# Kernel tuning notes

Hardware: AMD Instinct MI355X
Metric: run time of the kernel (lower is better)

## Reference

```python
import jax, jax.numpy as jnp
import numpy as np

EPS = 1e-3  # keras BatchNormalization default epsilon
NUM_HEADS = 8


def conv1d_same(x, w, b):
    # x: [B,T,Cin], w: [K,Cin,Cout]
    return jax.lax.conv_general_dilated(
        x, w, window_strides=(1,), padding='SAME',
        dimension_numbers=('NWC', 'WIO', 'NWC')) + b


def bn(x, g, b, m, v):
    # inference-mode batchnorm with moving stats
    return (x - m) * jax.lax.rsqrt(v + EPS) * g + b


def lstm(x, K, R, b):
    # x: [B,T,D] -> [B,T,U]; keras gate order i,f,c,o; recurrent_dropout off at inference
    B = x.shape[0]
    U = R.shape[0]
    xp = jnp.einsum('btd,dz->btz', x, K) + b  # precompute input projection

    def step(carry, xt):
        h, c = carry
        z = xt + h @ R
        i, f, g, o = jnp.split(z, 4, axis=-1)
        c = jax.nn.sigmoid(f) * c + jax.nn.sigmoid(i) * jnp.tanh(g)
        h = jax.nn.sigmoid(o) * jnp.tanh(c)
        return (h, c), h

    h0 = jnp.zeros((B, U), x.dtype)
    _, hs = jax.lax.scan(step, (h0, h0), jnp.swapaxes(xp, 0, 1))
    return jnp.swapaxes(hs, 0, 1)


def bilstm(x, Kf, Rf, bf, Kb, Rb, bb):
    fwd = lstm(x, Kf, Rf, bf)
    bwd = lstm(x[:, ::-1], Kb, Rb, bb)[:, ::-1]
    return jnp.concatenate([fwd, bwd], axis=-1)


def mhsa(x, wq, bq, wk, bk, wv, bv, wo, bo):
    B, T, _ = x.shape
    d_model = wq.shape[1]
    dh = d_model // NUM_HEADS
    q = (x @ wq + bq).reshape(B, T, NUM_HEADS, dh)
    k = (x @ wk + bk).reshape(B, T, NUM_HEADS, dh)
    v = (x @ wv + bv).reshape(B, T, NUM_HEADS, dh)
    logits = jnp.einsum('bqhd,bkhd->bhqk', q, k) / jnp.sqrt(jnp.asarray(dh, x.dtype))
    attn = jax.nn.softmax(logits, axis=-1)
    out = jnp.einsum('bhqk,bkhd->bqhd', attn, v).reshape(B, T, d_model)
    return out @ wo + bo


def setup_inputs() -> dict:
    key = jax.random.key(0)
    ks = iter(jax.random.split(key, 64))

    def nrm(shape, s=0.05):
        return (jax.random.normal(next(ks), shape) * s).astype(jnp.float32)

    p = {}
    p['x'] = jax.random.normal(next(ks), (512, 256, 78), dtype=jnp.float32)
    for name, shp in [
            ('conv5_w', (5, 78, 64)), ('conv7_w', (7, 78, 64)), ('conv9_w', (9, 78, 64)),
            ('fuse_w', (1, 192, 128)), ('se_w1', (128, 8)), ('se_w2', (8, 128)),
            ('l1f_k', (128, 512)), ('l1f_r', (128, 512)), ('l1b_k', (128, 512)), ('l1b_r', (128, 512)),
            ('l2f_k', (256, 256)), ('l2f_r', (64, 256)), ('l2b_k', (256, 256)), ('l2b_r', (64, 256)),
            ('wq', (128, 256)), ('wk', (128, 256)), ('wv', (128, 256)), ('wo', (256, 256)),
            ('d1_w', (256, 256)), ('d2_w', (256, 128)), ('d3_w', (128, 1)),
            ('conv5_b', (64,)), ('conv7_b', (64,)), ('conv9_b', (64,)), ('fuse_b', (128,)),
            ('se_b1', (8,)), ('se_b2', (128,)),
            ('l1f_b', (512,)), ('l1b_b', (512,)), ('l2f_b', (256,)), ('l2b_b', (256,)),
            ('bq', (256,)), ('bk', (256,)), ('bv', (256,)), ('bo', (256,)),
            ('d1_b', (256,)), ('d2_b', (128,)), ('d3_b', (1,))]:
        p[name] = nrm(shp)
    for tag, c in [('bn5', 64), ('bn7', 64), ('bn9', 64), ('bn_l1', 256),
                   ('bn_l2', 128), ('bn_d1', 256), ('bn_d2', 128)]:
        p[tag + '_g'] = jnp.ones((c,), jnp.float32)
        p[tag + '_b'] = jnp.zeros((c,), jnp.float32)
        p[tag + '_m'] = jnp.zeros((c,), jnp.float32)
        p[tag + '_v'] = jnp.ones((c,), jnp.float32)
    return p


def reference(x, conv5_w, conv5_b, bn5_g, bn5_b, bn5_m, bn5_v,
              conv7_w, conv7_b, bn7_g, bn7_b, bn7_m, bn7_v,
              conv9_w, conv9_b, bn9_g, bn9_b, bn9_m, bn9_v,
              fuse_w, fuse_b, se_w1, se_b1, se_w2, se_b2,
              l1f_k, l1f_r, l1f_b, l1b_k, l1b_r, l1b_b,
              bn_l1_g, bn_l1_b, bn_l1_m, bn_l1_v,
              l2f_k, l2f_r, l2f_b, l2b_k, l2b_r, l2b_b,
              bn_l2_g, bn_l2_b, bn_l2_m, bn_l2_v,
              wq, bq, wk, bk, wv, bv, wo, bo,
              d1_w, d1_b, bn_d1_g, bn_d1_b, bn_d1_m, bn_d1_v,
              d2_w, d2_b, bn_d2_g, bn_d2_b, bn_d2_m, bn_d2_v,
              d3_w, d3_b):
    def block(w, b, g, bt, m, v):
        h = jax.nn.relu(conv1d_same(x, w, b))
        h = bn(h, g, bt, m, v)
        B, T, C = h.shape  # MaxPooling1D(2, 'same'); T is even
        return h.reshape(B, T // 2, 2, C).max(axis=2)

    fused = jnp.concatenate([
        block(conv5_w, conv5_b, bn5_g, bn5_b, bn5_m, bn5_v),
        block(conv7_w, conv7_b, bn7_g, bn7_b, bn7_m, bn7_v),
        block(conv9_w, conv9_b, bn9_g, bn9_b, bn9_m, bn9_v)], axis=-1)
    fused = conv1d_same(fused, fuse_w, fuse_b)

    # SENet spatial attention
    s = fused.mean(axis=1)
    e = jax.nn.sigmoid(jax.nn.relu(s @ se_w1 + se_b1) @ se_w2 + se_b2)
    h = fused * e[:, None, :]

    h = bilstm(h, l1f_k, l1f_r, l1f_b, l1b_k, l1b_r, l1b_b)
    h = bn(h, bn_l1_g, bn_l1_b, bn_l1_m, bn_l1_v)
    h = bilstm(h, l2f_k, l2f_r, l2f_b, l2b_k, l2b_r, l2b_b)
    h = bn(h, bn_l2_g, bn_l2_b, bn_l2_m, bn_l2_v)

    h = mhsa(h, wq, bq, wk, bk, wv, bv, wo, bo)
    g_ = h.mean(axis=1)

    d = jax.nn.relu(g_ @ d1_w + d1_b)
    d = bn(d, bn_d1_g, bn_d1_b, bn_d1_m, bn_d1_v)
    d = jax.nn.relu(d @ d2_w + d2_b)
    d = bn(d, bn_d2_g, bn_d2_b, bn_d2_m, bn_d2_v)
    return jax.nn.sigmoid(d @ d3_w + d3_b)
```

## Files before the change

kernel.cpp:

```cpp
#include <hip/hip_runtime.h>

#define EPS 1e-3f

typedef __attribute__((ext_vector_type(8))) short bf16x8;
typedef __attribute__((ext_vector_type(4))) float f32x4;

__device__ __forceinline__ float sigm(float x){ return 1.0f/(1.0f + __expf(-x)); }
__device__ __forceinline__ float tanhfast(float x){ return 1.0f - 2.0f/(1.0f + __expf(2.0f*x)); }

__device__ __forceinline__ unsigned short f2b(float f){
    union { float f; unsigned u; } v; v.f = f;
    unsigned r = v.u + 0x7FFFu + ((v.u >> 16) & 1u);
    return (unsigned short)(r >> 16);
}
__device__ __forceinline__ float b2f(unsigned short h){
    union { unsigned u; float f; } v; v.u = ((unsigned)h) << 16; return v.f;
}

__global__ void __launch_bounds__(256)
prep_x(const float* __restrict__ x, unsigned short* __restrict__ xbf)
{
    const int b = blockIdx.x;
    const float* xs = x + (size_t)b*256*78;
    unsigned short* xd = xbf + (size_t)b*264*96;
    for (int p = threadIdx.x; p < 264*48; p += 256){
        int row = p / 48;
        int cp  = (p - row*48) * 2;
        int t   = row - 4;
        unsigned short v0 = 0, v1 = 0;
        if (t >= 0 && t < 256){
            if (cp   < 78) v0 = f2b(xs[t*78 + cp]);
            if (cp+1 < 78) v1 = f2b(xs[t*78 + cp + 1]);
        }
        *(unsigned int*)(xd + row*96 + cp) = (unsigned)v0 | ((unsigned)v1 << 16);
    }
}

__global__ void __launch_bounds__(256)
prep_w(const float* __restrict__ w5, const float* __restrict__ w7, const float* __restrict__ w9,
       unsigned short* __restrict__ wfrag)
{
    int g = blockIdx.x*256 + threadIdx.x;
    if (g >= 27*12*64) return;
    union { unsigned short s[8]; uint4 v; } u;
    int base = g * 8;
    #pragma unroll
    for (int e = 0; e < 8; ++e){
        int lin  = base + e;
        int slot = lin & 511;
        int fi   = lin >> 9;
        int nt   = fi % 12, kcs = fi / 12;
        int k    = kcs / 3, cs = kcs - k*3;
        int l15  = slot >> 5, r = slot & 31;
        int lg   = r >> 3, ee = r & 7;
        int ci   = cs*32 + lg*8 + ee;
        int co   = nt*16 + l15;
        float val = 0.f;
        if (ci < 78){
            if (co < 64){
                int kk = k - 2;
                if (kk >= 0 && kk < 5) val = w5[(kk*78 + ci)*64 + co];
            } else if (co < 128){
                int kk = k - 1;
                if (kk >= 0 && kk < 7) val = w7[(kk*78 + ci)*64 + (co - 64)];
            } else {
                val = w9[(k*78 + ci)*64 + (co - 128)];
            }
        }
        u.s[e] = f2b(val);
    }
    *(uint4*)(wfrag + base) = u.v;
}

__global__ void prep_ss(const float* b5, const float* b7, const float* b9,
                        const float* g5, const float* be5, const float* m5, const float* v5,
                        const float* g7, const float* be7, const float* m7, const float* v7,
                        const float* g9, const float* be9, const float* m9, const float* v9,
                        float* __restrict__ biascat, float* __restrict__ scale, float* __restrict__ shift)
{
    int c = threadIdx.x;
    if (c >= 192) return;
    float bv, g, be, m, v;
    if (c < 64){        bv=b5[c];      g=g5[c];      be=be5[c];      m=m5[c];      v=v5[c]; }
    else if (c < 128){  int i=c-64;  bv=b7[i]; g=g7[i]; be=be7[i]; m=m7[i]; v=v7[i]; }
    else {              int i=c-128; bv=b9[i]; g=g9[i]; be=be9[i]; m=m9[i]; v=v9[i]; }
    float s = g * rsqrtf(v + EPS);
    biascat[c] = bv;
    scale[c]   = s;
    shift[c]   = be - m*s;
}

__global__ void __launch_bounds__(256)
conv_mfma(const unsigned short* __restrict__ xbf,
          const unsigned short* __restrict__ wfrag,
          const float* __restrict__ biascat, const float* __restrict__ scale,
          const float* __restrict__ shift,
          float* __restrict__ out)
{
    const int b = blockIdx.x, tile = blockIdx.y;
    const int tid = threadIdx.x, lane = tid & 63, wv = tid >> 6;
    const int l15 = lane & 15, lg = lane >> 4;
    const int nt0 = wv * 3;
    const int t0  = tile * 64;

    f32x4 acc[4][3];
    #pragma unroll
    for (int nt = 0; nt < 3; ++nt){
        float bv = biascat[(nt0 + nt)*16 + l15];
        #pragma unroll
        for (int mt = 0; mt < 4; ++mt)
            acc[mt][nt] = (f32x4){bv, bv, bv, bv};
    }

    const unsigned short* xb = xbf + ((size_t)b*264 + t0 + l15)*96 + lg*8;
    const unsigned short* wb = wfrag + (size_t)nt0*512 + l15*32 + lg*8;

    for (int k = 0; k < 9; ++k){
        #pragma unroll
        for (int cs = 0; cs < 3; ++cs){
            bf16x8 A[4], Bf[3];
            #pragma unroll
            for (int mt = 0; mt < 4; ++mt)
                A[mt] = *(const bf16x8*)(xb + (size_t)(k + mt*16)*96 + cs*32);
            #pragma unroll
            for (int nt = 0; nt < 3; ++nt)
                Bf[nt] = *(const bf16x8*)(wb + (size_t)((k*3 + cs)*12 + nt)*512);
            #pragma unroll
            for (int mt = 0; mt < 4; ++mt)
                #pragma unroll
                for (int nt = 0; nt < 3; ++nt)
                    acc[mt][nt] = __builtin_amdgcn_mfma_f32_16x16x32_bf16(A[mt], Bf[nt], acc[mt][nt], 0, 0, 0);
        }
    }

    #pragma unroll
    for (int nt = 0; nt < 3; ++nt){
        int col = (nt0 + nt)*16 + l15;
        float s = scale[col], sh = shift[col];
        #pragma unroll
        for (int mt = 0; mt < 4; ++mt){
            float v0 = fmaxf(acc[mt][nt][0], 0.f)*s + sh;
            float v1 = fmaxf(acc[mt][nt][1], 0.f)*s + sh;
            float v2 = fmaxf(acc[mt][nt][2], 0.f)*s + sh;
            float v3 = fmaxf(acc[mt][nt][3], 0.f)*s + sh;
            int tb = tile*32 + mt*8 + lg*2;
            out[((size_t)b*128 + tb    )*192 + col] = fmaxf(v0, v1);
            out[((size_t)b*128 + tb + 1)*192 + col] = fmaxf(v2, v3);
        }
    }
}

__global__ void __launch_bounds__(128)
se_mean(const unsigned short* __restrict__ fb,
        const float* __restrict__ w1, const float* __restrict__ b1,
        const float* __restrict__ w2, const float* __restrict__ b2,
        float* __restrict__ e)
{
    int b = blockIdx.x, c = threadIdx.x;
    __shared__ float sv[128];
    __shared__ float rv[8];
    const unsigned short* fp = fb + (size_t)b*128*128 + c;
    float acc = 0.f;
    for (int t = 0; t < 128; ++t) acc += b2f(fp[t*128]);
    sv[c] = acc * (1.f/128.f);
    __syncthreads();
    if (c < 8){
        float r = b1[c];
        for (int i = 0; i < 128; ++i) r = fmaf(sv[i], w1[i*8 + c], r);
        rv[c] = fmaxf(r, 0.f);
    }
    __syncthreads();
    float ev = b2[c];
    #pragma unroll
    for (int j = 0; j < 8; ++j) ev = fmaf(rv[j], w2[j*128 + c], ev);
    e[(size_t)b*128 + c] = sigm(ev);
}

template<int K, bool ABF16, int OUTMODE, bool ESCALE>
__global__ void __launch_bounds__(256)
xp_gemm(const void* __restrict__ Av, const float* __restrict__ W,
        const float* __restrict__ bias, const float* __restrict__ esc,
        unsigned short* __restrict__ outp, int N)
{
    __shared__ unsigned short Asm[128][40];
    __shared__ unsigned short Bsm[8][64][8];
    __shared__ float esm[ESCALE ? K : 1];

    const int tid  = threadIdx.x;
    const int lane = tid & 63;
    const int wv   = tid >> 6;
    const int wm   = wv & 1;
    const int wn   = wv >> 1;
    const size_t m0 = (size_t)blockIdx.x * 128;
    const int n0   = blockIdx.y * 128;

    if constexpr (ESCALE){
        for (int i = tid; i < K; i += 256) esm[i] = esc[(size_t)blockIdx.x*K + i];
    }

    f32x4 acc[4][4];
    #pragma unroll
    for (int nt = 0; nt < 4; ++nt){
        float bv = bias[n0 + wn*64 + nt*16 + (lane & 15)];
        #pragma unroll
        for (int mt = 0; mt < 4; ++mt)
            acc[mt][nt] = (f32x4){bv, bv, bv, bv};
    }

    const int bn = tid & 127;
    const int bg = tid >> 7;

    for (int k0 = 0; k0 < K; k0 += 32){
        __syncthreads();
        if constexpr (!ABF16){
            const float* Ag = (const float*)Av;
            #pragma unroll
            for (int i = 0; i < 2; ++i){
                int g = tid + i*256;
                int r = g >> 2, c8 = g & 3;
                float4 d0 = *(const float4*)(Ag + (m0 + r)*K + k0 + c8*8);
                float4 d1 = *(const float4*)(Ag + (m0 + r)*K + k0 + c8*8 + 4);
                union { unsigned short s[8]; uint4 v; } u;
                u.s[0]=f2b(d0.x); u.s[1]=f2b(d0.y); u.s[2]=f2b(d0.z); u.s[3]=f2b(d0.w);
                u.s[4]=f2b(d1.x); u.s[5]=f2b(d1.y); u.s[6]=f2b(d1.z); u.s[7]=f2b(d1.w);
                *(uint4*)&Asm[r][c8*8] = u.v;
            }
        } else {
            const unsigned short* Ag = (const unsigned short*)Av;
            #pragma unroll
            for (int i = 0; i < 2; ++i){
                int g = tid + i*256;
                int r = g >> 2, c8 = g & 3;
                uint4 d = *(const uint4*)(Ag + (m0 + r)*K + k0 + c8*8);
                if constexpr (ESCALE){
                    unsigned short* s = (unsigned short*)&d;
                    #pragma unroll
                    for (int j = 0; j < 8; ++j)
                        s[j] = f2b(b2f(s[j]) * esm[k0 + c8*8 + j]);
                }
                *(uint4*)&Asm[r][c8*8] = d;
            }
        }
        {
            union { unsigned short s[8]; uint4 v; } u0, u1;
            #pragma unroll
            for (int q = 0; q < 8; ++q){
                u0.s[q] = f2b(W[(size_t)(k0 + bg*16 + q)*N + n0 + bn]);
                u1.s[q] = f2b(W[(size_t)(k0 + bg*16 + 8 + q)*N + n0 + bn]);
            }
            int nt = bn >> 4, lo = bn & 15;
            *(uint4*)&Bsm[nt][lo + 16*(2*bg)][0]   = u0.v;
            *(uint4*)&Bsm[nt][lo + 16*(2*bg+1)][0] = u1.v;
        }
        __syncthreads();

        bf16x8 af[4], bfr[4];
        #pragma unroll
        for (int mt = 0; mt < 4; ++mt)
            af[mt] = *(const bf16x8*)&Asm[wm*64 + mt*16 + (lane & 15)][(lane >> 4)*8];
        #pragma unroll
        for (int nt = 0; nt < 4; ++nt)
            bfr[nt] = *(const bf16x8*)&Bsm[wn*4 + nt][lane][0];
        #pragma unroll
        for (int mt = 0; mt < 4; ++mt)
            #pragma unroll
            for (int nt = 0; nt < 4; ++nt)
                acc[mt][nt] = __builtin_amdgcn_mfma_f32_16x16x32_bf16(af[mt], bfr[nt], acc[mt][nt], 0, 0, 0);
    }

    #pragma unroll
    for (int mt = 0; mt < 4; ++mt)
        #pragma unroll
        for (int nt = 0; nt < 4; ++nt)
            #pragma unroll
            for (int r = 0; r < 4; ++r){
                size_t row = m0 + wm*64 + mt*16 + (lane >> 4)*4 + r;
                int    col = n0 + wn*64 + nt*16 + (lane & 15);
                if constexpr (OUTMODE == 0){
                    outp[row*N + col] = f2b(acc[mt][nt][r]);
                } else if constexpr (OUTMODE == 1){
                    size_t off = ((size_t)((row >> 7)*8 + (col >> 5))*32 + (col & 31))*128 + (row & 127);
                    outp[off] = f2b(acc[mt][nt][r]);
                } else {
                    const int U = N/4;
                    outp[row*N + (col & (U-1))*4 + (col / U)] = f2b(acc[mt][nt][r]);
                }
            }
}

template<int U, bool OUT_BF16>
__global__ void __launch_bounds__(4*U, 4)
lstm_rec2(const unsigned short* __restrict__ xpf, const unsigned short* __restrict__ xpb,
          const float* __restrict__ Rf, const float* __restrict__ Rb,
          const float* __restrict__ bng, const float* __restrict__ bnb,
          const float* __restrict__ bnm, const float* __restrict__ bnv,
          void* __restrict__ outv)
{
    constexpr int Z  = 4*U;
    constexpr int KT = U/32;
    constexpr int HP = U + 8;

    __shared__ unsigned short h_lds[2][16][HP];

    const int tid = threadIdx.x, lane = tid & 63, wv = tid >> 6;
    const int l15 = lane & 15, lg = lane >> 4;
    const int dir = blockIdx.y;
    const int b0  = blockIdx.x * 4;

    const unsigned short* xp = dir ? xpb : xpf;
    const float* Rg = dir ? Rb : Rf;

    for (int i = tid; i < 2*16*HP; i += 4*U) ((unsigned short*)h_lds)[i] = 0;

    bf16x8 rf[KT][4];
    #pragma unroll
    for (int kt = 0; kt < KT; ++kt)
        #pragma unroll
        for (int g = 0; g < 4; ++g){
            union { unsigned short s[8]; bf16x8 v; } u;
            #pragma unroll
            for (int e = 0; e < 8; ++e)
                u.s[e] = f2b(Rg[(size_t)(kt*32 + lg*8 + e)*Z + g*U + wv*16 + l15]);
            rf[kt][g] = u.v;
        }

    const int u_ = wv*16 + l15;
    const bool glane = (lg == 0);
    const int ch = dir*U + u_;
    float bns = 0.f, bnsh = 0.f;
    if (glane){
        bns  = bng[ch] * rsqrtf(bnv[ch] + EPS);
        bnsh = bnb[ch] - bnm[ch]*bns;
    }
    float cst[4] = {0.f, 0.f, 0.f, 0.f};
    const unsigned short* xbase = xp + (size_t)b0*128*Z + u_*4;

    ushort4 xq[4] = {};
    if (glane){
        const int tf = dir ? 127 : 0;
        #pragma unroll
        for (int r = 0; r < 4; ++r)
            xq[r] = *(const ushort4*)(xbase + (size_t)r*128*Z + (size_t)tf*Z);
    }
    __syncthreads();

    int buf = 0;
    for (int ts = 0; ts < 128; ++ts){
        const int t = dir ? 127 - ts : ts;
        ushort4 xn[4] = {};
        if (glane && ts < 127){
            const int tn = dir ? t - 1 : t + 1;
            #pragma unroll
            for (int r = 0; r < 4; ++r)
                xn[r] = *(const ushort4*)(xbase + (size_t)r*128*Z + (size_t)tn*Z);
        }
        bf16x8 af[KT];
        #pragma unroll
        for (int kt = 0; kt < KT; ++kt)
            af[kt] = *(const bf16x8*)&h_lds[buf][l15][kt*32 + lg*8];
        f32x4 acc[4];
        #pragma unroll
        for (int g = 0; g < 4; ++g) acc[g] = (f32x4){0.f,0.f,0.f,0.f};
        #pragma unroll
        for (int kt = 0; kt < KT; ++kt)
            #pragma unroll
            for (int g = 0; g < 4; ++g)
                acc[g] = __builtin_amdgcn_mfma_f32_16x16x32_bf16(af[kt], rf[kt][g], acc[g], 0, 0, 0);
        if (glane){
            #pragma unroll
            for (int r = 0; r < 4; ++r){
                float zi = acc[0][r] + b2f(xq[r].x);
                float zf = acc[1][r] + b2f(xq[r].y);
                float zg = acc[2][r] + b2f(xq[r].z);
                float zo = acc[3][r] + b2f(xq[r].w);
                float c  = sigm(zf)*cst[r] + sigm(zi)*tanhfast(zg);
                cst[r] = c;
                float h = sigm(zo)*tanhfast(c);
                h_lds[buf^1][r][u_] = f2b(h);
                float hb = fmaf(h, bns, bnsh);
                size_t oidx = ((size_t)(b0 + r)*128 + t)*(size_t)(2*U) + ch;
                if constexpr (OUT_BF16) ((unsigned short*)outv)[oidx] = f2b(hb);
                else                    ((float*)outv)[oidx] = hb;
            }
        }
        __syncthreads();
        buf ^= 1;
        #pragma unroll
        for (int r = 0; r < 4; ++r) xq[r] = xn[r];
    }
}

__global__ void __launch_bounds__(256)
attn_kernel(const unsigned short* __restrict__ qb,
            const unsigned short* __restrict__ kb,
            const unsigned short* __restrict__ vb,
            float* __restrict__ msum)
{
    __shared__ unsigned short p_lds[128][136];
    __shared__ float red[4][2][16];

    const int b  = blockIdx.x, hd = blockIdx.y;
    const int tid = threadIdx.x, lane = tid & 63, wv = tid >> 6;
    const int m0 = wv * 32;
    const int l15 = lane & 15, lg = lane >> 4;

    bf16x8 aq[2];
    #pragma unroll
    for (int mt = 0; mt < 2; ++mt)
        aq[mt] = *(const bf16x8*)(qb + ((size_t)(b*128 + m0 + mt*16 + l15))*256 + hd*32 + lg*8);

    bf16x8 bk[8];
    #pragma unroll
    for (int nt = 0; nt < 8; ++nt)
        bk[nt] = *(const bf16x8*)(kb + ((size_t)(b*128 + nt*16 + l15))*256 + hd*32 + lg*8);

    f32x4 s[2][8];
    #pragma unroll
    for (int mt = 0; mt < 2; ++mt)
        #pragma unroll
        for (int nt = 0; nt < 8; ++nt) s[mt][nt] = (f32x4){0.f,0.f,0.f,0.f};
    #pragma unroll
    for (int mt = 0; mt < 2; ++mt)
        #pragma unroll
        for (int nt = 0; nt < 8; ++nt)
            s[mt][nt] = __builtin_amdgcn_mfma_f32_16x16x32_bf16(aq[mt], bk[nt], s[mt][nt], 0, 0, 0);

    const float scale = 0.17677669529663687f;
    #pragma unroll
    for (int mt = 0; mt < 2; ++mt)
        #pragma unroll
        for (int r = 0; r < 4; ++r){
            float mx = -1e30f;
            #pragma unroll
            for (int nt = 0; nt < 8; ++nt) mx = fmaxf(mx, s[mt][nt][r]);
            #pragma unroll
            for (int msk = 1; msk < 16; msk <<= 1) mx = fmaxf(mx, __shfl_xor(mx, msk, 64));
            float pv[8], sum = 0.f;
            #pragma unroll
            for (int nt = 0; nt < 8; ++nt){
                pv[nt] = __expf((s[mt][nt][r] - mx) * scale);
                sum += pv[nt];
            }
            #pragma unroll
            for (int msk = 1; msk < 16; msk <<= 1) sum += __shfl_xor(sum, msk, 64);
            float inv = 1.f / sum;
            int row = m0 + mt*16 + lg*4 + r;
            #pragma unroll
            for (int nt = 0; nt < 8; ++nt)
                p_lds[row][nt*16 + l15] = f2b(pv[nt] * inv);
        }
    __syncthreads();

    f32x4 o[2][2];
    #pragma unroll
    for (int mt = 0; mt < 2; ++mt)
        #pragma unroll
        for (int dn = 0; dn < 2; ++dn) o[mt][dn] = (f32x4){0.f,0.f,0.f,0.f};
    bf16x8 bv[4][2];
    #pragma unroll
    for (int kt = 0; kt < 4; ++kt)
        #pragma unroll
        for (int dn = 0; dn < 2; ++dn)
            bv[kt][dn] = *(const bf16x8*)(vb + ((size_t)(b*8 + hd)*32 + dn*16 + l15)*128 + kt*32 + lg*8);
    #pragma unroll
    for (int mt = 0; mt < 2; ++mt)
        #pragma unroll
        for (int kt = 0; kt < 4; ++kt){
            bf16x8 ap = *(const bf16x8*)&p_lds[m0 + mt*16 + l15][kt*32 + lg*8];
            #pragma unroll
            for (int dn = 0; dn < 2; ++dn)
                o[mt][dn] = __builtin_amdgcn_mfma_f32_16x16x32_bf16(ap, bv[kt][dn], o[mt][dn], 0, 0, 0);
        }

    float sm[2];
    #pragma unroll
    for (int dn = 0; dn < 2; ++dn){
        float a = 0.f;
        #pragma unroll
        for (int mt = 0; mt < 2; ++mt)
            #pragma unroll
            for (int r = 0; r < 4; ++r) a += o[mt][dn][r];
        a += __shfl_xor(a, 16, 64);
        a += __shfl_xor(a, 32, 64);
        sm[dn] = a;
    }
    if (lg == 0){
        red[wv][0][l15] = sm[0];
        red[wv][1][l15] = sm[1];
    }
    __syncthreads();
    if (tid < 32){
        int dn = tid >> 4, n = tid & 15;
        float tot = red[0][dn][n] + red[1][dn][n] + red[2][dn][n] + red[3][dn][n];
        msum[(size_t)b*256 + hd*32 + dn*16 + n] = tot * (1.f/128.f);
    }
}

__global__ void __launch_bounds__(256)
head_kernel(const float* __restrict__ msum,
            const float* __restrict__ wo, const float* __restrict__ bo,
            const float* __restrict__ d1w, const float* __restrict__ d1b,
            const float* __restrict__ g1, const float* __restrict__ b1,
            const float* __restrict__ m1, const float* __restrict__ v1,
            const float* __restrict__ d2w, const float* __restrict__ d2b,
            const float* __restrict__ g2, const float* __restrict__ b2,
            const float* __restrict__ m2, const float* __restrict__ v2,
            const float* __restrict__ d3w, const float* __restrict__ d3b,
            float* __restrict__ outp)
{
    int b = blockIdx.x, j = threadIdx.x;
    __shared__ float s1[256];
    __shared__ float s2[256];
    const float* mr = msum + (size_t)b*256;
    float acc = bo[j];
    #pragma unroll 4
    for (int i = 0; i < 256; ++i) acc = fmaf(mr[i], wo[i*256 + j], acc);
    s1[j] = acc;
    __syncthreads();
    float a1 = d1b[j];
    #pragma unroll 4
    for (int i = 0; i < 256; ++i) a1 = fmaf(s1[i], d1w[i*256 + j], a1);
    a1 = fmaxf(a1, 0.f);
    float sc1 = g1[j] * rsqrtf(v1[j] + EPS);
    a1 = a1 * sc1 + (b1[j] - m1[j] * sc1);
    s2[j] = a1;
    __syncthreads();
    if (j < 128){
        float a2 = d2b[j];
        #pragma unroll 4
        for (int i = 0; i < 256; ++i) a2 = fmaf(s2[i], d2w[i*128 + j], a2);
        a2 = fmaxf(a2, 0.f);
        float sc2 = g2[j] * rsqrtf(v2[j] + EPS);
        a2 = a2 * sc2 + (b2[j] - m2[j] * sc2);
        s1[j] = a2;
    }
    __syncthreads();
    if (j == 0){
        float a3 = d3b[0];
        for (int i = 0; i < 128; ++i) a3 = fmaf(s1[i], d3w[i], a3);
        outp[b] = sigm(a3);
    }
}

extern "C" void kernel_launch(void* const* d_in, const int* in_sizes, int n_in,
                              void* d_out, int out_size, void* d_ws, size_t ws_size,
                              hipStream_t stream)
{
    #define F(i) ((const float*)d_in[i])
    const float* x       = F(0);
    const float* conv5_w = F(1);
    const float* conv7_w = F(2);
    const float* conv9_w = F(3);
    const float* fuse_w  = F(4);
    const float* se_w1   = F(5);
    const float* se_w2   = F(6);
    const float* l1f_k   = F(7);
    const float* l1f_r   = F(8);
    const float* l1b_k   = F(9);
    const float* l1b_r   = F(10);
    const float* l2f_k   = F(11);
    const float* l2f_r   = F(12);
    const float* l2b_k   = F(13);
    const float* l2b_r   = F(14);
    const float* wq      = F(15);
    const float* wk      = F(16);
    const float* wv      = F(17);
    const float* wo      = F(18);
    const float* d1_w    = F(19);
    const float* d2_w    = F(20);
    const float* d3_w    = F(21);
    const float* conv5_b = F(22);
    const float* conv7_b = F(23);
    const float* conv9_b = F(24);
    const float* fuse_b  = F(25);
    const float* se_b1   = F(26);
    const float* se_b2   = F(27);
    const float* l1f_b   = F(28);
    const float* l1b_b   = F(29);
    const float* l2f_b   = F(30);
    const float* l2b_b   = F(31);
    const float* bq      = F(32);
    const float* bk      = F(33);
    const float* bv      = F(34);
    const float* bo      = F(35);
    const float* d1_b    = F(36);
    const float* d2_b    = F(37);
    const float* d3_b    = F(38);
    const float* bn5_g = F(39), *bn5_b = F(40), *bn5_m = F(41), *bn5_v = F(42);
    const float* bn7_g = F(43), *bn7_b = F(44), *bn7_m = F(45), *bn7_v = F(46);
    const float* bn9_g = F(47), *bn9_b = F(48), *bn9_m = F(49), *bn9_v = F(50);
    const float* bnl1_g = F(51), *bnl1_b = F(52), *bnl1_m = F(53), *bnl1_v = F(54);
    const float* bnl2_g = F(55), *bnl2_b = F(56), *bnl2_m = F(57), *bnl2_v = F(58);
    const float* bnd1_g = F(59), *bnd1_b = F(60), *bnd1_m = F(61), *bnd1_v = F(62);
    const float* bnd2_g = F(63), *bnd2_b = F(64), *bnd2_m = F(65), *bnd2_v = F(66);
    #undef F

    float* ws = (float*)d_ws;
    float* concat = ws;
    unsigned short* fusedbf = (unsigned short*)(ws + 12582912);
    float* e      = ws + 16777216;
    unsigned short* xbf   = (unsigned short*)(ws + 20971520);
    unsigned short* wfrag = (unsigned short*)(ws + 27607040);
    float* biascat = ws + 27689984;
    float* cscale  = ws + 27690176;
    float* cshift  = ws + 27690368;
    unsigned short* xp1f  = (unsigned short*)(ws);
    unsigned short* xp1b  = (unsigned short*)(ws + 20971520);
    unsigned short* l1out = (unsigned short*)(ws + 29360128);
    unsigned short* xp2f  = (unsigned short*)(ws);
    unsigned short* xp2b  = (unsigned short*)(ws + 4194304);
    unsigned short* l2out = (unsigned short*)(ws + 8388608);
    unsigned short* qbuf  = (unsigned short*)(ws + 12582912);
    unsigned short* kbuf  = (unsigned short*)(ws);
    unsigned short* vbuf  = (unsigned short*)(ws + 20971520);
    float* msum   = ws + 29360128;
    float* outp   = (float*)d_out;

    prep_x<<<dim3(512), dim3(256), 0, stream>>>(x, xbf);
    prep_w<<<dim3(81), dim3(256), 0, stream>>>(conv5_w, conv7_w, conv9_w, wfrag);
    prep_ss<<<dim3(1), dim3(192), 0, stream>>>(
        conv5_b, conv7_b, conv9_b,
        bn5_g, bn5_b, bn5_m, bn5_v,
        bn7_g, bn7_b, bn7_m, bn7_v,
        bn9_g, bn9_b, bn9_m, bn9_v,
        biascat, cscale, cshift);
    conv_mfma<<<dim3(512,4), dim3(256), 0, stream>>>(
        xbf, wfrag, biascat, cscale, cshift, concat);

    xp_gemm<192,false,0,false><<<dim3(512,1), dim3(256), 0, stream>>>(
        concat, fuse_w, fuse_b, nullptr, fusedbf, 128);
    se_mean<<<dim3(512), dim3(128), 0, stream>>>(fusedbf, se_w1, se_b1, se_w2, se_b2, e);

    xp_gemm<128,true,2,true><<<dim3(512,4), dim3(256), 0, stream>>>(
        fusedbf, l1f_k, l1f_b, e, xp1f, 512);
    xp_gemm<128,true,2,true><<<dim3(512,4), dim3(256), 0, stream>>>(
        fusedbf, l1b_k, l1b_b, e, xp1b, 512);
    lstm_rec2<128,true><<<dim3(128,2), dim3(512), 0, stream>>>(
        xp1f, xp1b, l1f_r, l1b_r, bnl1_g, bnl1_b, bnl1_m, bnl1_v, l1out);

    xp_gemm<256,true,2,false><<<dim3(512,2), dim3(256), 0, stream>>>(
        l1out, l2f_k, l2f_b, nullptr, xp2f, 256);
    xp_gemm<256,true,2,false><<<dim3(512,2), dim3(256), 0, stream>>>(
        l1out, l2b_k, l2b_b, nullptr, xp2b, 256);
    lstm_rec2<64,true><<<dim3(128,2), dim3(256), 0, stream>>>(
        xp2f, xp2b, l2f_r, l2b_r, bnl2_g, bnl2_b, bnl2_m, bnl2_v, l2out);

    xp_gemm<128,true,0,false><<<dim3(512,2), dim3(256), 0, stream>>>(
        l2out, wq, bq, nullptr, qbuf, 256);
    xp_gemm<128,true,0,false><<<dim3(512,2), dim3(256), 0, stream>>>(
        l2out, wk, bk, nullptr, kbuf, 256);
    xp_gemm<128,true,1,false><<<dim3(512,2), dim3(256), 0, stream>>>(
        l2out, wv, bv, nullptr, vbuf, 256);

    attn_kernel<<<dim3(512,8), dim3(256), 0, stream>>>(qbuf, kbuf, vbuf, msum);

    head_kernel<<<dim3(512), dim3(256), 0, stream>>>(
        msum, wo, bo,
        d1_w, d1_b, bnd1_g, bnd1_b, bnd1_m, bnd1_v,
        d2_w, d2_b, bnd2_g, bnd2_b, bnd2_m, bnd2_v,
        d3_w, d3_b, outp);

    (void)in_sizes; (void)n_in; (void)out_size; (void)ws_size;
}
```

Before: 861.9 us.

## Pack 16 batch rows per LSTM recurrence block using all MFMA output rows

The recurrent LSTM kernel now processes 16 batch sequences per block instead of 4. The 16x16 MFMA tile's M dimension is fully used, and all four lane groups do gate math rather than only one. The grid shrinks from 128 to 32 blocks per direction, which cuts redundant MFMA work per sequence. The trade-off is far fewer blocks, 64 in total, on a GPU with many CUs, and more per-lane work in each serial timestep.

```diff
diff --git a/kernel.cpp b/kernel.cpp
--- a/kernel.cpp
+++ b/kernel.cpp
@@ -289,8 +289,8 @@
 }
 
 template<int U, bool OUT_BF16>
-__global__ void __launch_bounds__(4*U, 4)
-lstm_rec2(const unsigned short* __restrict__ xpf, const unsigned short* __restrict__ xpb,
+__global__ void __launch_bounds__(4*U)
+lstm_rec3(const unsigned short* __restrict__ xpf, const unsigned short* __restrict__ xpb,
           const float* __restrict__ Rf, const float* __restrict__ Rb,
           const float* __restrict__ bng, const float* __restrict__ bnb,
           const float* __restrict__ bnm, const float* __restrict__ bnv,
@@ -305,7 +305,7 @@
     const int tid = threadIdx.x, lane = tid & 63, wv = tid >> 6;
     const int l15 = lane & 15, lg = lane >> 4;
     const int dir = blockIdx.y;
-    const int b0  = blockIdx.x * 4;
+    const int b0  = blockIdx.x * 16;
 
     const unsigned short* xp = dir ? xpb : xpf;
     const float* Rg = dir ? Rb : Rf;
@@ -325,22 +325,18 @@
         }
 
     const int u_ = wv*16 + l15;
-    const bool glane = (lg == 0);
     const int ch = dir*U + u_;
-    float bns = 0.f, bnsh = 0.f;
-    if (glane){
-        bns  = bng[ch] * rsqrtf(bnv[ch] + EPS);
-        bnsh = bnb[ch] - bnm[ch]*bns;
-    }
+    const float bns  = bng[ch] * rsqrtf(bnv[ch] + EPS);
+    const float bnsh = bnb[ch] - bnm[ch]*bns;
     float cst[4] = {0.f, 0.f, 0.f, 0.f};
-    const unsigned short* xbase = xp + (size_t)b0*128*Z + u_*4;
-
-    ushort4 xq[4] = {};
-    if (glane){
+    const unsigned short* xbase = xp + ((size_t)(b0 + lg*4)*128)*Z + u_*4;
+
+    ushort4 xq[4];
+    {
         const int tf = dir ? 127 : 0;
         #pragma unroll
         for (int r = 0; r < 4; ++r)
-            xq[r] = *(const ushort4*)(xbase + (size_t)r*128*Z + (size_t)tf*Z);
+            xq[r] = *(const ushort4*)(xbase + ((size_t)r*128 + tf)*Z);
     }
     __syncthreads();
 
@@ -348,11 +344,11 @@
     for (int ts = 0; ts < 128; ++ts){
         const int t = dir ? 127 - ts : ts;
         ushort4 xn[4] = {};
-        if (glane && ts < 127){
+        if (ts < 127){
             const int tn = dir ? t - 1 : t + 1;
             #pragma unroll
             for (int r = 0; r < 4; ++r)
-                xn[r] = *(const ushort4*)(xbase + (size_t)r*128*Z + (size_t)tn*Z);
+                xn[r] = *(const ushort4*)(xbase + ((size_t)r*128 + tn)*Z);
         }
         bf16x8 af[KT];
         #pragma unroll
@@ -366,22 +362,20 @@
             #pragma unroll
             for (int g = 0; g < 4; ++g)
                 acc[g] = __builtin_amdgcn_mfma_f32_16x16x32_bf16(af[kt], rf[kt][g], acc[g], 0, 0, 0);
-        if (glane){
-            #pragma unroll
-            for (int r = 0; r < 4; ++r){
-                float zi = acc[0][r] + b2f(xq[r].x);
-                float zf = acc[1][r] + b2f(xq[r].y);
-                float zg = acc[2][r] + b2f(xq[r].z);
-                float zo = acc[3][r] + b2f(xq[r].w);
-                float c  = sigm(zf)*cst[r] + sigm(zi)*tanhfast(zg);
-                cst[r] = c;
-                float h = sigm(zo)*tanhfast(c);
-                h_lds[buf^1][r][u_] = f2b(h);
-                float hb = fmaf(h, bns, bnsh);
-                size_t oidx = ((size_t)(b0 + r)*128 + t)*(size_t)(2*U) + ch;
-                if constexpr (OUT_BF16) ((unsigned short*)outv)[oidx] = f2b(hb);
-                else                    ((float*)outv)[oidx] = hb;
-            }
+        #pragma unroll
+        for (int r = 0; r < 4; ++r){
+            float zi = acc[0][r] + b2f(xq[r].x);
+            float zf = acc[1][r] + b2f(xq[r].y);
+            float zg = acc[2][r] + b2f(xq[r].z);
+            float zo = acc[3][r] + b2f(xq[r].w);
+            float c  = sigm(zf)*cst[r] + sigm(zi)*tanhfast(zg);
+            cst[r] = c;
+            float h = sigm(zo)*tanhfast(c);
+            h_lds[buf^1][lg*4 + r][u_] = f2b(h);
+            float hb = fmaf(h, bns, bnsh);
+            size_t oidx = ((size_t)(b0 + lg*4 + r)*128 + t)*(size_t)(2*U) + ch;
+            if constexpr (OUT_BF16) ((unsigned short*)outv)[oidx] = f2b(hb);
+            else                    ((float*)outv)[oidx] = hb;
         }
         __syncthreads();
         buf ^= 1;
@@ -635,14 +629,14 @@
         fusedbf, l1f_k, l1f_b, e, xp1f, 512);
     xp_gemm<128,true,2,true><<<dim3(512,4), dim3(256), 0, stream>>>(
         fusedbf, l1b_k, l1b_b, e, xp1b, 512);
-    lstm_rec2<128,true><<<dim3(128,2), dim3(512), 0, stream>>>(
+    lstm_rec3<128,true><<<dim3(32,2), dim3(512), 0, stream>>>(
         xp1f, xp1b, l1f_r, l1b_r, bnl1_g, bnl1_b, bnl1_m, bnl1_v, l1out);
 
     xp_gemm<256,true,2,false><<<dim3(512,2), dim3(256), 0, stream>>>(
         l1out, l2f_k, l2f_b, nullptr, xp2f, 256);
     xp_gemm<256,true,2,false><<<dim3(512,2), dim3(256), 0, stream>>>(
         l1out, l2b_k, l2b_b, nullptr, xp2b, 256);
-    lstm_rec2<64,true><<<dim3(128,2), dim3(256), 0, stream>>>(
+    lstm_rec3<64,true><<<dim3(32,2), dim3(256), 0, stream>>>(
         xp2f, xp2b, l2f_r, l2b_r, bnl2_g, bnl2_b, bnl2_m, bnl2_v, l2out);
 
     xp_gemm<128,true,0,false><<<dim3(512,2), dim3(256), 0, stream>>>(
```

Result: no change. 858.7 us (-0.4%).
